# Kernel tuning notes

Hardware: AMD Instinct MI355X
Metric: run time of the kernel (lower is better)

## Reference

```python
import jax, jax.numpy as jnp
import numpy as np

B, S, E, H = 4, 1024, 1024, 16
D = E // H  # head_dim = 64
SCALE = float(np.sqrt(D))


def setup_inputs() -> dict:
    key = jax.random.key(0)
    ks = jax.random.split(key, 12)
    lim = 1.0 / np.sqrt(E)  # torch nn.Linear default init range

    def lin(kw, kb):
        W = jax.random.uniform(kw, (E, E), jnp.float32, -lim, lim)
        b = jax.random.uniform(kb, (E,), jnp.float32, -lim, lim)
        return W, b

    W0, b0 = lin(ks[0], ks[1])
    W1, b1 = lin(ks[2], ks[3])
    W2, b2 = lin(ks[4], ks[5])
    Wv, bv = lin(ks[6], ks[7])
    Wo, bo = lin(ks[8], ks[9])
    A = jax.random.normal(ks[10], (D, D, D), jnp.float32)  # torch.randn core tensor
    x = jax.random.normal(ks[11], (B, S, E), jnp.float32)
    return {"x": x, "W0": W0, "b0": b0, "W1": W1, "b1": b1, "W2": W2, "b2": b2,
            "Wv": Wv, "bv": bv, "Wo": Wo, "bo": bo, "A": A}


def _heads(h):
    # (B,S,E) -> (B,H,S,D)
    return h.reshape(B, S, H, D).transpose(0, 2, 1, 3)


def reference(x, W0, b0, W1, b1, W2, b2, Wv, bv, Wo, bo, A):
    p0 = _heads(x @ W0.T + b0)
    p1 = _heads(x @ W1.T + b1)
    p2 = _heads(x @ W2.T + b2)
    # N=3 multilinear attention score: third projection is contracted over its
    # own sequence index k (faithful to the original einsum construction).
    logits = jnp.einsum('acd,bhia,bhjc,bhkd->bhij', A, p0, p1, p2,
                        optimize=True) / SCALE  # (B,H,S,S)
    attn = jax.nn.softmax(logits, axis=-1)  # dropout inactive (eval / p=0)
    v = _heads(x @ Wv.T + bv)
    values = jnp.einsum('bhij,bhjd->bhid', attn, v)  # (B,H,S,D)
    values = values.transpose(0, 2, 1, 3).reshape(B, S, E)
    out = values @ Wo.T + bo
    return out, attn
```

## Files before the change

kernel.cpp:

```cpp
#include <hip/hip_runtime.h>
#include <hip/hip_bf16.h>
#include <cstddef>

#define B_ 4
#define S_ 1024
#define E_ 1024
#define H_ 16
#define D_ 64
#define BH_ (B_*H_)

typedef __attribute__((ext_vector_type(8))) short short8;
typedef __attribute__((ext_vector_type(4))) float f32x4;
typedef __attribute__((ext_vector_type(4))) unsigned short us4;
typedef unsigned short u16;

__device__ inline u16 f2b(float x) {
    return __builtin_bit_cast(u16, __float2bfloat16(x));
}
__device__ inline float b2f(u16 u) {
    return __bfloat162float(__builtin_bit_cast(__hip_bfloat16, u));
}
__device__ inline void splitf(float x, u16& h, u16& l) {
    h = f2b(x); l = f2b(x - b2f(h));
}

__device__ inline void split_one(const float* __restrict__ in,
                                 u16* __restrict__ oh, u16* __restrict__ ol, int i)
{
    float4 v = ((const float4*)in)[i];
    us4 h, l;
    splitf(v.x, ((u16*)&h)[0], ((u16*)&l)[0]);
    splitf(v.y, ((u16*)&h)[1], ((u16*)&l)[1]);
    splitf(v.z, ((u16*)&h)[2], ((u16*)&l)[2]);
    splitf(v.w, ((u16*)&h)[3], ((u16*)&l)[3]);
    ((us4*)oh)[i] = h;
    ((us4*)ol)[i] = l;
}

__device__ inline void conv_one(const float* __restrict__ in,
                                u16* __restrict__ ob, int i)
{
    float4 v = ((const float4*)in)[i];
    us4 h;
    ((u16*)&h)[0] = f2b(v.x); ((u16*)&h)[1] = f2b(v.y);
    ((u16*)&h)[2] = f2b(v.z); ((u16*)&h)[3] = f2b(v.w);
    ((us4*)ob)[i] = h;
}

__global__ __launch_bounds__(256) void prep(
    const float* __restrict__ x, const float* __restrict__ W0,
    const float* __restrict__ W1, const float* __restrict__ Wv,
    const float* __restrict__ Wo, float* __restrict__ xsum_p,
    u16* __restrict__ xh, u16* __restrict__ xl,
    u16* __restrict__ w0h, u16* __restrict__ w0l,
    u16* __restrict__ w1h, u16* __restrict__ w1l,
    u16* __restrict__ wvb, u16* __restrict__ wob)
{
    int bid = blockIdx.x, tid = threadIdx.x;
    if (bid < 4096) {
        split_one(x, xh, xl, bid * 256 + tid);
    } else if (bid < 5120) {
        split_one(W0, w0h, w0l, (bid - 4096) * 256 + tid);
    } else if (bid < 6144) {
        split_one(W1, w1h, w1l, (bid - 5120) * 256 + tid);
    } else if (bid < 7168) {
        conv_one(Wv, wvb, (bid - 6144) * 256 + tid);
    } else if (bid < 8192) {
        conv_one(Wo, wob, (bid - 7168) * 256 + tid);
    } else {
        int p = bid - 8192;
        int kb = p & 3, b = (p >> 2) & 3, ch = p >> 4;
        int k = kb * 256 + tid;
        const float* base = x + ((size_t)(b * S_ + ch * 64)) * E_ + k;
        float s = 0.f;
#pragma unroll 8
        for (int j = 0; j < 64; ++j) s += base[(size_t)j * E_];
        xsum_p[(ch * 4 + b) * E_ + k] = s;
    }
}

__global__ __launch_bounds__(256) void t2k_M(
    const float* __restrict__ W2, const float* __restrict__ b2v,
    const float* __restrict__ xsum_p, const float* __restrict__ A,
    u16* __restrict__ MTh, u16* __restrict__ MTl)
{
    int h = blockIdx.x, b = blockIdx.y, tid = threadIdx.x;
    __shared__ float xs[1024];
    __shared__ float t2s[64];

#pragma unroll
    for (int j = 0; j < 4; ++j) {
        int k = j * 256 + tid;
        float s = 0.f;
#pragma unroll
        for (int c = 0; c < 16; ++c) s += xsum_p[(c * 4 + b) * E_ + k];
        xs[k] = s;
    }
    __syncthreads();

    int w = tid >> 6, lane = tid & 63;
    for (int nn = w; nn < 64; nn += 4) {
        int n = h * 64 + nn;
        const float* wr = W2 + (size_t)n * E_;
        float s = 0.f;
#pragma unroll
        for (int t = 0; t < 16; ++t) s = fmaf(wr[t * 64 + lane], xs[t * 64 + lane], s);
#pragma unroll
        for (int off = 1; off < 64; off <<= 1) s += __shfl_xor(s, off, 64);
        if (lane == 0) t2s[nn] = s + 1024.0f * b2v[n];
    }
    __syncthreads();

    int bh = b * H_ + h;
    int c = tid & 63;
    int a0 = (tid >> 6) * 16;
    for (int a = a0; a < a0 + 16; ++a) {
        float s = 0.f;
        const float* Ap = A + ((size_t)a * 64 + c) * 64;
#pragma unroll 8
        for (int d = 0; d < 64; ++d) s = fmaf(Ap[d], t2s[d], s);
        u16 hh, ll; splitf(s * 0.125f, hh, ll);
        MTh[(size_t)bh * 4096 + c * 64 + a] = hh;
        MTl[(size_t)bh * 4096 + c * 64 + a] = ll;
    }
}

__device__ void qp1_body(
    const u16* __restrict__ Xh, const u16* __restrict__ Xl,
    const u16* __restrict__ W0h_, const u16* __restrict__ W0l_,
    const u16* __restrict__ W1h_, const u16* __restrict__ W1l_,
    const float* __restrict__ bias0, const float* __restrict__ bias1,
    const u16* __restrict__ MTh, const u16* __restrict__ MTl,
    u16* __restrict__ qh, u16* __restrict__ ql,
    u16* __restrict__ p1h, u16* __restrict__ p1l,
    int bm, int bn, char* smem)
{
    const int K = 1024;
    u16* Xs_h  = (u16*)smem;
    u16* Xs_l  = Xs_h + 128 * 40;
    u16* W0s_h = Xs_l + 128 * 40;
    u16* W0s_l = W0s_h + 64 * 40;
    u16* W1s_h = W0s_l + 64 * 40;
    u16* W1s_l = W1s_h + 64 * 40;
    u16* Cs_h  = (u16*)smem;
    u16* Cs_l  = Cs_h + 128 * 72;

    const int tid = threadIdx.x;
    const int w = tid >> 6, lane = tid & 63;
    const int waveM = w & 1, waveN = w >> 1;
    const int quad = lane >> 4, l16 = lane & 15;

    const int xrow = tid >> 1, xko = (tid & 1) * 16;
    const int wrow = tid >> 2, wko = (tid & 3) * 8;

    const u16* xh_g  = Xh  + (size_t)(bm * 128 + xrow) * K + xko;
    const u16* xl_g  = Xl  + (size_t)(bm * 128 + xrow) * K + xko;
    const u16* w0h_g = W0h_ + (size_t)(bn * 64 + wrow) * K + wko;
    const u16* w0l_g = W0l_ + (size_t)(bn * 64 + wrow) * K + wko;
    const u16* w1h_g = W1h_ + (size_t)(bn * 64 + wrow) * K + wko;
    const u16* w1l_g = W1l_ + (size_t)(bn * 64 + wrow) * K + wko;

    f32x4 acc0[4][2] = {};
    f32x4 acc1[4][2] = {};

    for (int k0 = 0; k0 < K; k0 += 32) {
        uint4 xa = *(const uint4*)(xh_g + k0);
        uint4 xb = *(const uint4*)(xh_g + k0 + 8);
        uint4 xc = *(const uint4*)(xl_g + k0);
        uint4 xd = *(const uint4*)(xl_g + k0 + 8);
        uint4 w0a = *(const uint4*)(w0h_g + k0);
        uint4 w0c = *(const uint4*)(w0l_g + k0);
        uint4 w1a = *(const uint4*)(w1h_g + k0);
        uint4 w1c = *(const uint4*)(w1l_g + k0);
        __syncthreads();
        *(uint4*)&Xs_h[xrow * 40 + xko]     = xa;
        *(uint4*)&Xs_h[xrow * 40 + xko + 8] = xb;
        *(uint4*)&Xs_l[xrow * 40 + xko]     = xc;
        *(uint4*)&Xs_l[xrow * 40 + xko + 8] = xd;
        *(uint4*)&W0s_h[wrow * 40 + wko] = w0a;
        *(uint4*)&W0s_l[wrow * 40 + wko] = w0c;
        *(uint4*)&W1s_h[wrow * 40 + wko] = w1a;
        *(uint4*)&W1s_l[wrow * 40 + wko] = w1c;
        __syncthreads();

        short8 ah[4], al[4], b0h[2], b0l[2], b1h[2], b1l[2];
#pragma unroll
        for (int mt = 0; mt < 4; ++mt) {
            int r = (waveM * 64 + mt * 16 + l16) * 40 + quad * 8;
            ah[mt] = *(short8*)&Xs_h[r];
            al[mt] = *(short8*)&Xs_l[r];
        }
#pragma unroll
        for (int nt = 0; nt < 2; ++nt) {
            int r = (waveN * 32 + nt * 16 + l16) * 40 + quad * 8;
            b0h[nt] = *(short8*)&W0s_h[r];
            b0l[nt] = *(short8*)&W0s_l[r];
            b1h[nt] = *(short8*)&W1s_h[r];
            b1l[nt] = *(short8*)&W1s_l[r];
        }
#pragma unroll
        for (int mt = 0; mt < 4; ++mt)
#pragma unroll
            for (int nt = 0; nt < 2; ++nt) {
                acc0[mt][nt] = __builtin_amdgcn_mfma_f32_16x16x32_bf16(ah[mt], b0h[nt], acc0[mt][nt], 0, 0, 0);
                acc1[mt][nt] = __builtin_amdgcn_mfma_f32_16x16x32_bf16(ah[mt], b1h[nt], acc1[mt][nt], 0, 0, 0);
                acc0[mt][nt] = __builtin_amdgcn_mfma_f32_16x16x32_bf16(ah[mt], b0l[nt], acc0[mt][nt], 0, 0, 0);
                acc1[mt][nt] = __builtin_amdgcn_mfma_f32_16x16x32_bf16(ah[mt], b1l[nt], acc1[mt][nt], 0, 0, 0);
                acc0[mt][nt] = __builtin_amdgcn_mfma_f32_16x16x32_bf16(al[mt], b0h[nt], acc0[mt][nt], 0, 0, 0);
                acc1[mt][nt] = __builtin_amdgcn_mfma_f32_16x16x32_bf16(al[mt], b1h[nt], acc1[mt][nt], 0, 0, 0);
            }
    }

    const int bh = (bm >> 3) * H_ + bn;

#pragma unroll
    for (int mt = 0; mt < 4; ++mt)
#pragma unroll
        for (int nt = 0; nt < 2; ++nt)
#pragma unroll
            for (int r = 0; r < 4; ++r) {
                int m = bm * 128 + waveM * 64 + mt * 16 + quad * 4 + r;
                int n = bn * 64 + waveN * 32 + nt * 16 + l16;
                float val = acc1[mt][nt][r] + bias1[n];
                int s = m & 1023, c = n & 63;
                size_t addr = ((size_t)bh * S_ + s) * 64 + c;
                u16 hh, ll; splitf(val, hh, ll);
                p1h[addr] = hh; p1l[addr] = ll;
            }

    __syncthreads();
#pragma unroll
    for (int mt = 0; mt < 4; ++mt)
#pragma unroll
        for (int nt = 0; nt < 2; ++nt)
#pragma unroll
            for (int r = 0; r < 4; ++r) {
                int i = waveM * 64 + mt * 16 + quad * 4 + r;
                int a = waveN * 32 + nt * 16 + l16;
                float val = acc0[mt][nt][r] + bias0[bn * 64 + a];
                u16 hh, ll; splitf(val, hh, ll);
                Cs_h[i * 72 + a] = hh;
                Cs_l[i * 72 + a] = ll;
            }
    __syncthreads();

    const u16* MTh_b = MTh + (size_t)bh * 4096;
    const u16* MTl_b = MTl + (size_t)bh * 4096;
    f32x4 qacc[4][2] = {};
#pragma unroll
    for (int ch = 0; ch < 2; ++ch) {
        short8 mh[2], ml[2];
#pragma unroll
        for (int nt = 0; nt < 2; ++nt) {
            int c = waveN * 32 + nt * 16 + l16;
            mh[nt] = *(const short8*)&MTh_b[c * 64 + ch * 32 + quad * 8];
            ml[nt] = *(const short8*)&MTl_b[c * 64 + ch * 32 + quad * 8];
        }
#pragma unroll
        for (int mt = 0; mt < 4; ++mt) {
            int rr = (waveM * 64 + mt * 16 + l16) * 72 + ch * 32 + quad * 8;
            short8 ca = *(short8*)&Cs_h[rr];
            short8 cl = *(short8*)&Cs_l[rr];
#pragma unroll
            for (int nt = 0; nt < 2; ++nt) {
                qacc[mt][nt] = __builtin_amdgcn_mfma_f32_16x16x32_bf16(ca, mh[nt], qacc[mt][nt], 0, 0, 0);
                qacc[mt][nt] = __builtin_amdgcn_mfma_f32_16x16x32_bf16(ca, ml[nt], qacc[mt][nt], 0, 0, 0);
                qacc[mt][nt] = __builtin_amdgcn_mfma_f32_16x16x32_bf16(cl, mh[nt], qacc[mt][nt], 0, 0, 0);
            }
        }
    }
#pragma unroll
    for (int mt = 0; mt < 4; ++mt)
#pragma unroll
        for (int nt = 0; nt < 2; ++nt)
#pragma unroll
            for (int r = 0; r < 4; ++r) {
                int s = (bm & 7) * 128 + waveM * 64 + mt * 16 + quad * 4 + r;
                int c = waveN * 32 + nt * 16 + l16;
                size_t addr = ((size_t)bh * S_ + s) * 64 + c;
                u16 hh, ll; splitf(qacc[mt][nt][r], hh, ll);
                qh[addr] = hh; ql[addr] = ll;
            }
}

__device__ void plain128_body(
    const u16* __restrict__ Xb, const u16* __restrict__ Wb,
    const float* __restrict__ bias, u16* __restrict__ outB,
    float* __restrict__ outF, int mode, int bm, int bn, char* smem)
{
    const int K = 1024;
    u16* Xs = (u16*)smem;
    u16* Ws = Xs + 128 * 40;

    const int tid = threadIdx.x;
    const int w = tid >> 6, lane = tid & 63;
    const int waveM = w & 1, waveN = w >> 1;
    const int quad = lane >> 4, l16 = lane & 15;
    const int xrow = tid >> 1, xko = (tid & 1) * 16;
    const int wrow = tid >> 2, wko = (tid & 3) * 8;

    const u16* xg = Xb + (size_t)(bm * 128 + xrow) * K + xko;
    const u16* wg = Wb + (size_t)(bn * 64 + wrow) * K + wko;

    f32x4 acc[4][2] = {};

    for (int k0 = 0; k0 < K; k0 += 32) {
        uint4 xa = *(const uint4*)(xg + k0);
        uint4 xb = *(const uint4*)(xg + k0 + 8);
        uint4 wa = *(const uint4*)(wg + k0);
        __syncthreads();
        *(uint4*)&Xs[xrow * 40 + xko]     = xa;
        *(uint4*)&Xs[xrow * 40 + xko + 8] = xb;
        *(uint4*)&Ws[wrow * 40 + wko]     = wa;
        __syncthreads();

        short8 af[4], bf_[2];
#pragma unroll
        for (int mt = 0; mt < 4; ++mt)
            af[mt] = *(short8*)&Xs[(waveM * 64 + mt * 16 + l16) * 40 + quad * 8];
#pragma unroll
        for (int nt = 0; nt < 2; ++nt)
            bf_[nt] = *(short8*)&Ws[(waveN * 32 + nt * 16 + l16) * 40 + quad * 8];
#pragma unroll
        for (int mt = 0; mt < 4; ++mt)
#pragma unroll
            for (int nt = 0; nt < 2; ++nt)
                acc[mt][nt] = __builtin_amdgcn_mfma_f32_16x16x32_bf16(af[mt], bf_[nt], acc[mt][nt], 0, 0, 0);
    }

#pragma unroll
    for (int mt = 0; mt < 4; ++mt)
#pragma unroll
        for (int nt = 0; nt < 2; ++nt)
#pragma unroll
            for (int r = 0; r < 4; ++r) {
                int m = bm * 128 + waveM * 64 + mt * 16 + quad * 4 + r;
                int n = bn * 64 + waveN * 32 + nt * 16 + l16;
                float val = acc[mt][nt][r] + bias[n];
                if (mode == 0) {
                    int b = m >> 10, s = m & 1023, h = n >> 6, c = n & 63;
                    outB[((size_t)((b * H_ + h) * 64 + c)) * S_ + s] = f2b(val);
                } else {
                    outF[(size_t)m * 1024 + n] = val;
                }
            }
}

__global__ __launch_bounds__(256) void gemm_mid(
    const u16* __restrict__ xh, const u16* __restrict__ xl,
    const u16* __restrict__ w0h, const u16* __restrict__ w0l,
    const u16* __restrict__ w1h, const u16* __restrict__ w1l,
    const float* __restrict__ b0, const float* __restrict__ b1,
    const u16* __restrict__ MTh, const u16* __restrict__ MTl,
    u16* __restrict__ qh, u16* __restrict__ ql,
    u16* __restrict__ p1h, u16* __restrict__ p1l,
    const u16* __restrict__ wvb, const float* __restrict__ bv,
    u16* __restrict__ vT)
{
    __shared__ __align__(16) char smem[40960];
    int bid = blockIdx.x;
    if (bid < 512) {
        qp1_body(xh, xl, w0h, w0l, w1h, w1l, b0, b1, MTh, MTl,
                 qh, ql, p1h, p1l, bid & 31, bid >> 5, smem);
    } else {
        int b2 = bid - 512;
        plain128_body(xh, wvb, bv, vT, nullptr, 0, b2 & 31, b2 >> 5, smem);
    }
}

__global__ __launch_bounds__(256) void gemm_fin(
    const u16* __restrict__ values, const u16* __restrict__ wob,
    const float* __restrict__ bo, float* __restrict__ out)
{
    __shared__ __align__(16) char smem[15360];
    plain128_body(values, wob, bo, nullptr, out, 1, blockIdx.x, blockIdx.y, smem);
}

__global__ __launch_bounds__(512) void logits_softmax_pv(
    const u16* __restrict__ qh, const u16* __restrict__ ql,
    const u16* __restrict__ p1h, const u16* __restrict__ p1l,
    const u16* __restrict__ vT, float* __restrict__ attn,
    u16* __restrict__ values)
{
    int bh = blockIdx.x, i0 = blockIdx.y * 32;
    int b = bh >> 4, h = bh & 15;
    int tid = threadIdx.x, w = tid >> 6, lane = tid & 63;
    int quad = lane >> 4, l16 = lane & 15;
    int wg = w >> 2, wj = w & 3;

    __shared__ __align__(16) char sm[56320];
    u16* qhs  = (u16*)sm;
    u16* qls  = (u16*)(sm + 4608);
    u16* p1hs = (u16*)(sm + 9216);
    u16* p1ls = (u16*)(sm + 27648);
    float* redm = (float*)(sm + 55296);
    float* reds = (float*)(sm + 55808);
    u16* Ps  = (u16*)sm;
    u16* vs_ = (u16*)(sm + 18432);

    {
        int row = tid >> 4, c0 = (tid & 15) * 4;
        size_t g = ((size_t)bh * S_ + i0 + row) * 64 + c0;
        *(us4*)&qhs[row * 72 + c0] = *(const us4*)&qh[g];
        *(us4*)&qls[row * 72 + c0] = *(const us4*)&ql[g];
    }

    const int jl = tid >> 3, c0s = (tid & 7) * 8;
    const size_t gp = ((size_t)bh * S_ + jl) * 64 + c0s;

    uint4 rha = *(const uint4*)&p1h[gp];
    uint4 rla = *(const uint4*)&p1l[gp];
    *(uint4*)&p1hs[jl * 72 + c0s] = rha;
    *(uint4*)&p1ls[jl * 72 + c0s] = rla;
    uint4 rh1 = *(const uint4*)&p1h[gp + 4096];
    uint4 rl1 = *(const uint4*)&p1l[gp + 4096];
    __syncthreads();

    short8 ah[2], al[2];
#pragma unroll
    for (int ch = 0; ch < 2; ++ch) {
        ah[ch] = *(short8*)&qhs[(wg * 16 + l16) * 72 + ch * 32 + quad * 8];
        al[ch] = *(short8*)&qls[(wg * 16 + l16) * 72 + ch * 32 + quad * 8];
    }

    f32x4 L[16];
    for (int t = 0; t < 16; ++t) {
        int cur = t & 1;
        uint4 rh2, rl2;
        if (t < 14) {
            size_t gn = gp + (size_t)(t + 2) * 4096;
            rh2 = *(const uint4*)&p1h[gn];
            rl2 = *(const uint4*)&p1l[gn];
        }
        int jr = wj * 16 + l16;
        const u16* Hb = &p1hs[cur * 4608 + jr * 72];
        const u16* Lb = &p1ls[cur * 4608 + jr * 72];
        short8 bh0 = *(const short8*)(Hb + quad * 8);
        short8 bh1 = *(const short8*)(Hb + 32 + quad * 8);
        short8 bl0 = *(const short8*)(Lb + quad * 8);
        short8 bl1 = *(const short8*)(Lb + 32 + quad * 8);
        f32x4 a = {};
        a = __builtin_amdgcn_mfma_f32_16x16x32_bf16(ah[0], bh0, a, 0, 0, 0);
        a = __builtin_amdgcn_mfma_f32_16x16x32_bf16(ah[1], bh1, a, 0, 0, 0);
        a = __builtin_amdgcn_mfma_f32_16x16x32_bf16(ah[0], bl0, a, 0, 0, 0);
        a = __builtin_amdgcn_mfma_f32_16x16x32_bf16(ah[1], bl1, a, 0, 0, 0);
        a = __builtin_amdgcn_mfma_f32_16x16x32_bf16(al[0], bh0, a, 0, 0, 0);
        a = __builtin_amdgcn_mfma_f32_16x16x32_bf16(al[1], bh1, a, 0, 0, 0);
        L[t] = a;
        if (t < 15) {
            *(uint4*)&p1hs[(1 - cur) * 4608 + jl * 72 + c0s] = rh1;
            *(uint4*)&p1ls[(1 - cur) * 4608 + jl * 72 + c0s] = rl1;
            if (t < 14) { rh1 = rh2; rl1 = rl2; }
            __syncthreads();
        }
    }

    float mrow[4], srow[4];
#pragma unroll
    for (int r = 0; r < 4; ++r) {
        float m = L[0][r];
#pragma unroll
        for (int t = 1; t < 16; ++t) m = fmaxf(m, L[t][r]);
#pragma unroll
        for (int off = 1; off < 16; off <<= 1) m = fmaxf(m, __shfl_xor(m, off, 64));
        mrow[r] = m;
    }
    if (l16 == 0)
#pragma unroll
        for (int r = 0; r < 4; ++r) redm[wj * 32 + wg * 16 + quad * 4 + r] = mrow[r];
    __syncthreads();
#pragma unroll
    for (int r = 0; r < 4; ++r) {
        int rowg = wg * 16 + quad * 4 + r;
        float m = fmaxf(fmaxf(redm[0 * 32 + rowg], redm[1 * 32 + rowg]),
                        fmaxf(redm[2 * 32 + rowg], redm[3 * 32 + rowg]));
        float s = 0.f;
#pragma unroll
        for (int t = 0; t < 16; ++t) { L[t][r] = __expf(L[t][r] - m); s += L[t][r]; }
#pragma unroll
        for (int off = 1; off < 16; off <<= 1) s += __shfl_xor(s, off, 64);
        srow[r] = s;
    }
    if (l16 == 0)
#pragma unroll
        for (int r = 0; r < 4; ++r) reds[wj * 32 + wg * 16 + quad * 4 + r] = srow[r];
    __syncthreads();
#pragma unroll
    for (int r = 0; r < 4; ++r) {
        int rowg = wg * 16 + quad * 4 + r;
        float inv = 1.0f / (reds[0 * 32 + rowg] + reds[1 * 32 + rowg] +
                            reds[2 * 32 + rowg] + reds[3 * 32 + rowg]);
        float* arow = attn + ((size_t)bh * S_ + i0 + rowg) * S_;
#pragma unroll
        for (int t = 0; t < 16; ++t) {
            float p = L[t][r] * inv;
            L[t][r] = p;
            __builtin_nontemporal_store(p, &arow[t * 64 + wj * 16 + l16]);
        }
    }

    const int dv = tid >> 3, jc = (tid & 7) * 8;
    const size_t gv = (size_t)(bh * 64 + dv) * S_;
    uint4 rv0 = *(const uint4*)&vT[gv + jc];
    uint4 rv1 = *(const uint4*)&vT[gv + 64 + jc];

    f32x4 acc_pv = {};
    const int d = wj * 16 + l16;
    for (int tt = 0; tt < 8; ++tt) {
        int cur = tt & 1;
        u16* Pb = Ps + cur * 4608;
        u16* Vb = vs_ + cur * 9216;
#pragma unroll
        for (int r = 0; r < 4; ++r) {
            int pr = (wg * 16 + quad * 4 + r) * 72 + wj * 16 + l16;
            Pb[pr]        = f2b(L[2 * tt][r]);
            Pb[2304 + pr] = f2b(L[2 * tt + 1][r]);
        }
        *(uint4*)&Vb[dv * 72 + jc]        = rv0;
        *(uint4*)&Vb[4608 + dv * 72 + jc] = rv1;
        __syncthreads();
        if (tt < 7) {
            rv0 = *(const uint4*)&vT[gv + (size_t)(2 * tt + 2) * 64 + jc];
            rv1 = *(const uint4*)&vT[gv + (size_t)(2 * tt + 3) * 64 + jc];
        }
#pragma unroll
        for (int tp = 0; tp < 2; ++tp)
#pragma unroll
            for (int cc = 0; cc < 64; cc += 32) {
                short8 af = *(short8*)&Pb[tp * 2304 + (wg * 16 + l16) * 72 + cc + quad * 8];
                short8 bf = *(short8*)&Vb[tp * 4608 + d * 72 + cc + quad * 8];
                acc_pv = __builtin_amdgcn_mfma_f32_16x16x32_bf16(af, bf, acc_pv, 0, 0, 0);
            }
    }
#pragma unroll
    for (int r = 0; r < 4; ++r) {
        int i = i0 + wg * 16 + quad * 4 + r;
        values[((size_t)(b * S_ + i)) * E_ + h * 64 + d] = f2b(acc_pv[r]);
    }
}

extern "C" void kernel_launch(void* const* d_in, const int* in_sizes, int n_in,
                              void* d_out, int out_size, void* d_ws, size_t ws_size,
                              hipStream_t stream)
{
    const float* x  = (const float*)d_in[0];
    const float* W0 = (const float*)d_in[1];
    const float* b0 = (const float*)d_in[2];
    const float* W1 = (const float*)d_in[3];
    const float* b1 = (const float*)d_in[4];
    const float* W2 = (const float*)d_in[5];
    const float* b2 = (const float*)d_in[6];
    const float* Wv = (const float*)d_in[7];
    const float* bv = (const float*)d_in[8];
    const float* Wo = (const float*)d_in[9];
    const float* bo = (const float*)d_in[10];
    const float* A  = (const float*)d_in[11];

    float* out  = (float*)d_out;
    float* attn = out + (size_t)B_ * S_ * E_;

    u16* xh  = (u16*)d_ws;
    u16* xl  = xh + 4194304;
    u16* w0h = xl + 4194304;
    u16* w0l = w0h + 1048576;
    u16* w1h = w0l + 1048576;
    u16* w1l = w1h + 1048576;
    u16* p1h = w1l + 1048576;
    u16* p1l = p1h + 4194304;
    u16* qh  = p1l + 4194304;
    u16* ql  = qh + 4194304;
    u16* vT  = ql + 4194304;
    u16* values = vT + 4194304;
    u16* MTh = values + 4194304;
    u16* MTl = MTh + 262144;
    u16* wob = MTl + 262144;
    float* xsum_p = (float*)p1h;
    u16* wvb = values;

    prep<<<8448, 256, 0, stream>>>(x, W0, W1, Wv, Wo, xsum_p,
                                   xh, xl, w0h, w0l, w1h, w1l, wvb, wob);
    t2k_M<<<dim3(16, 4), 256, 0, stream>>>(W2, b2, xsum_p, A, MTh, MTl);

    gemm_mid<<<1024, 256, 0, stream>>>(xh, xl, w0h, w0l, w1h, w1l,
                                       b0, b1, MTh, MTl, qh, ql, p1h, p1l,
                                       wvb, bv, vT);

    logits_softmax_pv<<<dim3(64, 32), 512, 0, stream>>>(qh, ql, p1h, p1l, vT, attn, values);

    gemm_fin<<<dim3(32, 16), 256, 0, stream>>>(values, wob, bo, out);
}
```

Baseline: 537.7 us.

## Load MFMA operands directly from global, stage full P tile in swizzled LDS

The logits/softmax/PV kernel no longer double-buffers p1 and V tiles through shared memory. Each wave now loads its q, p1 and vT MFMA fragments straight from global memory, which removes the per-tile __syncthreads barriers. The full 32x1024 bf16 probability tile is written once into a 64KB XOR-swizzled LDS buffer and read back for the PV product. The trade-off is more redundant global/L2 traffic across waves, less latency hiding, and higher LDS use that may lower occupancy.

```diff
diff --git a/kernel.cpp b/kernel.cpp
--- a/kernel.cpp
+++ b/kernel.cpp
@@ -388,57 +388,28 @@
     int quad = lane >> 4, l16 = lane & 15;
     int wg = w >> 2, wj = w & 3;
 
-    __shared__ __align__(16) char sm[56320];
-    u16* qhs  = (u16*)sm;
-    u16* qls  = (u16*)(sm + 4608);
-    u16* p1hs = (u16*)(sm + 9216);
-    u16* p1ls = (u16*)(sm + 27648);
-    float* redm = (float*)(sm + 55296);
-    float* reds = (float*)(sm + 55808);
-    u16* Ps  = (u16*)sm;
-    u16* vs_ = (u16*)(sm + 18432);
-
+    __shared__ __align__(16) char sm[65536];
+    float* redm = (float*)sm;
+    float* reds = (float*)(sm + 512);
+
+    short8 ah[2], al[2];
     {
-        int row = tid >> 4, c0 = (tid & 15) * 4;
-        size_t g = ((size_t)bh * S_ + i0 + row) * 64 + c0;
-        *(us4*)&qhs[row * 72 + c0] = *(const us4*)&qh[g];
-        *(us4*)&qls[row * 72 + c0] = *(const us4*)&ql[g];
-    }
-
-    const int jl = tid >> 3, c0s = (tid & 7) * 8;
-    const size_t gp = ((size_t)bh * S_ + jl) * 64 + c0s;
-
-    uint4 rha = *(const uint4*)&p1h[gp];
-    uint4 rla = *(const uint4*)&p1l[gp];
-    *(uint4*)&p1hs[jl * 72 + c0s] = rha;
-    *(uint4*)&p1ls[jl * 72 + c0s] = rla;
-    uint4 rh1 = *(const uint4*)&p1h[gp + 4096];
-    uint4 rl1 = *(const uint4*)&p1l[gp + 4096];
-    __syncthreads();
-
-    short8 ah[2], al[2];
-#pragma unroll
-    for (int ch = 0; ch < 2; ++ch) {
-        ah[ch] = *(short8*)&qhs[(wg * 16 + l16) * 72 + ch * 32 + quad * 8];
-        al[ch] = *(short8*)&qls[(wg * 16 + l16) * 72 + ch * 32 + quad * 8];
-    }
-
+        size_t gq = ((size_t)bh * S_ + i0 + wg * 16 + l16) * 64 + quad * 8;
+        ah[0] = *(const short8*)&qh[gq];
+        ah[1] = *(const short8*)&qh[gq + 32];
+        al[0] = *(const short8*)&ql[gq];
+        al[1] = *(const short8*)&ql[gq + 32];
+    }
+
+    const size_t gpb = ((size_t)bh * S_ + wj * 16 + l16) * 64 + quad * 8;
     f32x4 L[16];
+#pragma unroll
     for (int t = 0; t < 16; ++t) {
-        int cur = t & 1;
-        uint4 rh2, rl2;
-        if (t < 14) {
-            size_t gn = gp + (size_t)(t + 2) * 4096;
-            rh2 = *(const uint4*)&p1h[gn];
-            rl2 = *(const uint4*)&p1l[gn];
-        }
-        int jr = wj * 16 + l16;
-        const u16* Hb = &p1hs[cur * 4608 + jr * 72];
-        const u16* Lb = &p1ls[cur * 4608 + jr * 72];
-        short8 bh0 = *(const short8*)(Hb + quad * 8);
-        short8 bh1 = *(const short8*)(Hb + 32 + quad * 8);
-        short8 bl0 = *(const short8*)(Lb + quad * 8);
-        short8 bl1 = *(const short8*)(Lb + 32 + quad * 8);
+        size_t g = gpb + (size_t)t * 4096;
+        short8 bh0 = *(const short8*)&p1h[g];
+        short8 bh1 = *(const short8*)&p1h[g + 32];
+        short8 bl0 = *(const short8*)&p1l[g];
+        short8 bl1 = *(const short8*)&p1l[g + 32];
         f32x4 a = {};
         a = __builtin_amdgcn_mfma_f32_16x16x32_bf16(ah[0], bh0, a, 0, 0, 0);
         a = __builtin_amdgcn_mfma_f32_16x16x32_bf16(ah[1], bh1, a, 0, 0, 0);
@@ -447,12 +418,6 @@
         a = __builtin_amdgcn_mfma_f32_16x16x32_bf16(al[0], bh0, a, 0, 0, 0);
         a = __builtin_amdgcn_mfma_f32_16x16x32_bf16(al[1], bh1, a, 0, 0, 0);
         L[t] = a;
-        if (t < 15) {
-            *(uint4*)&p1hs[(1 - cur) * 4608 + jl * 72 + c0s] = rh1;
-            *(uint4*)&p1ls[(1 - cur) * 4608 + jl * 72 + c0s] = rl1;
-            if (t < 14) { rh1 = rh2; rl1 = rl2; }
-            __syncthreads();
-        }
     }
 
     float mrow[4], srow[4];
@@ -499,39 +464,34 @@
         }
     }
 
-    const int dv = tid >> 3, jc = (tid & 7) * 8;
-    const size_t gv = (size_t)(bh * 64 + dv) * S_;
-    uint4 rv0 = *(const uint4*)&vT[gv + jc];
-    uint4 rv1 = *(const uint4*)&vT[gv + 64 + jc];
-
+    __syncthreads();
+    {
+        int row = wg * 16 + quad * 4;
+        int colb = (wj * 16 + l16) * 2;
+#pragma unroll
+        for (int t = 0; t < 16; ++t)
+#pragma unroll
+            for (int r = 0; r < 4; ++r) {
+                int off = (t * 128 + colb) ^ (((row + r) & 7) << 4);
+                *(u16*)(sm + (row + r) * 2048 + off) = f2b(L[t][r]);
+            }
+    }
+    __syncthreads();
+
+    const int d = wj * 16 + l16;
+    const int arow = wg * 16 + l16;
+    const char* Pr = sm + arow * 2048;
+    const int rxor = (arow & 7) << 4;
+    const size_t gvb = (size_t)(bh * 64 + d) * S_ + quad * 8;
     f32x4 acc_pv = {};
-    const int d = wj * 16 + l16;
-    for (int tt = 0; tt < 8; ++tt) {
-        int cur = tt & 1;
-        u16* Pb = Ps + cur * 4608;
-        u16* Vb = vs_ + cur * 9216;
-#pragma unroll
-        for (int r = 0; r < 4; ++r) {
-            int pr = (wg * 16 + quad * 4 + r) * 72 + wj * 16 + l16;
-            Pb[pr]        = f2b(L[2 * tt][r]);
-            Pb[2304 + pr] = f2b(L[2 * tt + 1][r]);
+#pragma unroll
+    for (int t = 0; t < 16; ++t)
+#pragma unroll
+        for (int cc = 0; cc < 64; cc += 32) {
+            short8 af = *(const short8*)(Pr + ((t * 128 + cc * 2 + quad * 16) ^ rxor));
+            short8 bf = *(const short8*)&vT[gvb + t * 64 + cc];
+            acc_pv = __builtin_amdgcn_mfma_f32_16x16x32_bf16(af, bf, acc_pv, 0, 0, 0);
         }
-        *(uint4*)&Vb[dv * 72 + jc]        = rv0;
-        *(uint4*)&Vb[4608 + dv * 72 + jc] = rv1;
-        __syncthreads();
-        if (tt < 7) {
-            rv0 = *(const uint4*)&vT[gv + (size_t)(2 * tt + 2) * 64 + jc];
-            rv1 = *(const uint4*)&vT[gv + (size_t)(2 * tt + 3) * 64 + jc];
-        }
-#pragma unroll
-        for (int tp = 0; tp < 2; ++tp)
-#pragma unroll
-            for (int cc = 0; cc < 64; cc += 32) {
-                short8 af = *(short8*)&Pb[tp * 2304 + (wg * 16 + l16) * 72 + cc + quad * 8];
-                short8 bf = *(short8*)&Vb[tp * 4608 + d * 72 + cc + quad * 8];
-                acc_pv = __builtin_amdgcn_mfma_f32_16x16x32_bf16(af, bf, acc_pv, 0, 0, 0);
-            }
-    }
 #pragma unroll
     for (int r = 0; r < 4; ++r) {
         int i = i0 + wg * 16 + quad * 4 + r;
```

Result: slower. 647.4 us (+20.4%).
